# Optimization experiments

Measured on AMD Instinct MI355X. Metric: run time of the kernel, lower is better.

## Reference

```python
import jax, jax.numpy as jnp
import numpy as np

N = 1024
IN_F = 128
H0 = 192  # num_features * 2
H1 = 96   # num_features * 1
BN_EPS = 1e-5
SLOPE = 0.01  # LeakyReLU default negative slope


def setup_inputs() -> dict:
    key = jax.random.key(0)
    ks = jax.random.split(key, 8)
    node_feat = jax.random.normal(ks[0], (N, IN_F), dtype=jnp.float32)
    W0 = jax.random.normal(ks[1], (H0, IN_F), dtype=jnp.float32) * 0.05
    g0 = jnp.ones((H0,), jnp.float32); b0 = jnp.zeros((H0,), jnp.float32)
    m0 = jnp.zeros((H0,), jnp.float32); v0 = jnp.ones((H0,), jnp.float32)
    W1 = jax.random.normal(ks[2], (H1, H0), dtype=jnp.float32) * 0.05
    g1 = jnp.ones((H1,), jnp.float32); b1 = jnp.zeros((H1,), jnp.float32)
    m1 = jnp.zeros((H1,), jnp.float32); v1 = jnp.ones((H1,), jnp.float32)
    Wout = jax.random.normal(ks[3], (1, H1), dtype=jnp.float32) * 0.05
    bout = jnp.zeros((1,), jnp.float32)
    return dict(node_feat=node_feat, W0=W0, g0=g0, b0=b0, m0=m0, v0=v0,
                W1=W1, g1=g1, b1=b1, m1=m1, v1=v1, Wout=Wout, bout=bout)


def _bn(x, g, b, m, v):
    # BatchNorm2d in eval mode over channel axis (last axis here)
    return (x - m) * (g * jax.lax.rsqrt(v + BN_EPS)) + b


def _leaky(x):
    return jnp.where(x >= 0, x, SLOPE * x)


def reference(node_feat, W0, g0, b0, m0, v0, W1, g1, b1, m1, v1, Wout, bout):
    n = node_feat.shape[0]
    # pairwise abs diff: [N, N, F] (symmetric, so torch's i/j transpose is a no-op)
    x_ij = jnp.abs(node_feat[:, None, :] - node_feat[None, :, :])
    # 1x1 convs == per-(i,j) matmuls over channel axis
    h = _leaky(_bn(jnp.einsum('ijf,cf->ijc', x_ij, W0), g0, b0, m0, v0))
    h = _leaky(_bn(jnp.einsum('ijc,dc->ijd', h, W1), g1, b1, m1, v1))
    logits = jnp.einsum('ijd,od->ijo', h, Wout)[..., 0] + bout[0]  # [N, N]
    sim_val = jax.nn.sigmoid(logits)
    edge = sim_val + jnp.eye(n, dtype=sim_val.dtype) + 1e-6
    # torch sums over dim=1 of [1, N, N] -> normalize over the row index i
    edge = edge / jnp.sum(edge, axis=0, keepdims=True)
    return edge[None], sim_val  # edge_feat [1, N, N], sim_val [N, N]
```

## Files before the change

kernel.cpp:

```cpp
#include <hip/hip_runtime.h>
#include <hip/hip_bf16.h>
#include <math.h>

typedef float v4f __attribute__((ext_vector_type(4)));
typedef __bf16 bf16x8 __attribute__((ext_vector_type(8)));
typedef __bf16 bf16x4 __attribute__((ext_vector_type(4)));

#define NN   1024
#define INF  128
#define H0C  192
#define H1C  96

#define WS_W0BF   0
#define WS_W1BF   49152
#define WS_BN0SW  86016
#define WS_BN1SW  86784
#define WS_WOUTSW 87168
#define WS_CINV   87552

__global__ __launch_bounds__(256) void prep_kernel(
    const float* __restrict__ W0, const float* __restrict__ g0,
    const float* __restrict__ b0, const float* __restrict__ m0,
    const float* __restrict__ v0, const float* __restrict__ W1,
    const float* __restrict__ g1, const float* __restrict__ b1,
    const float* __restrict__ m1, const float* __restrict__ v1,
    const float* __restrict__ Wout, char* __restrict__ ws)
{
    int e = blockIdx.x * 256 + threadIdx.x;
    __bf16* w0bf = (__bf16*)(ws + WS_W0BF);
    __bf16* w1bf = (__bf16*)(ws + WS_W1BF);
    float* bn0sw = (float*)(ws + WS_BN0SW);
    float* bn1sw = (float*)(ws + WS_BN1SW);
    float* woutsw = (float*)(ws + WS_WOUTSW);
    if (e < 24576) {
        int j = e & 7, lane = (e >> 3) & 63, t = e >> 9;
        int ks = t & 3, mt = t >> 2;
        int c = mt * 16 + (lane & 15);
        int k = ks * 32 + ((lane >> 4) << 3) + j;
        float s = g0[c] * rsqrtf(v0[c] + 1e-5f);
        w0bf[e] = (__bf16)(W0[c * INF + k] * s);
    } else if (e < 43008) {
        int e2 = e - 24576;
        int j = e2 & 7, lane = (e2 >> 3) & 63, t = e2 >> 9;
        int ks = t % 6, mt = t / 6;
        int c = mt * 16 + (lane & 15);
        int k = ks * 32 + ((lane >> 4) << 3) + j;
        float s = g1[c] * rsqrtf(v1[c] + 1e-5f);
        w1bf[e2] = (__bf16)(W1[c * H0C + k] * s);
    } else if (e < 43200) {
        int e3 = e - 43008;
        int q = e3 / 48, rem = e3 % 48, cm = rem >> 2, r = rem & 3;
        int c = cm * 16 + q * 4 + r;
        float s = g0[c] * rsqrtf(v0[c] + 1e-5f);
        bn0sw[e3] = b0[c] - m0[c] * s;
    } else if (e < 43296) {
        int e4 = e - 43200;
        int q = e4 / 24, rem = e4 % 24, mt = rem >> 2, r = rem & 3;
        int c = mt * 16 + q * 4 + r;
        float s = g1[c] * rsqrtf(v1[c] + 1e-5f);
        bn1sw[e4] = b1[c] - m1[c] * s;
    } else if (e < 43392) {
        int e5 = e - 43296;
        int q = e5 / 24, rem = e5 % 24, mt = rem >> 2, r = rem & 3;
        woutsw[e5] = Wout[mt * 16 + q * 4 + r];
    }
}

__global__ __launch_bounds__(256, 3) void edgenet_main(
    const float* __restrict__ feat, const char* __restrict__ ws,
    const float* __restrict__ boutp, float* __restrict__ sim_out)
{
    __shared__ __align__(16) char smem[51200];
    const int tid = threadIdx.x;
    const int lane = tid & 63;
    const int wave = tid >> 6;
    const int l16 = lane & 15;
    const int quad = lane >> 4;

    const int id = blockIdx.x;
    int bi = (int)((129.0f - sqrtf(16641.0f - 4.0f * (float)id)) * 0.5f);
    while (bi > 0 && bi * (129 - bi) > id) --bi;
    while ((bi + 1) * (128 - bi) <= id) ++bi;
    const int bj = 2 * bi + (id - bi * (129 - bi));
    const int i0 = bi << 4;
    const int j0 = bj << 3;
    const int jb = j0 + wave * 2;

    {
        int ii = tid & 15, fblk = tid >> 4;
        const float* fi = feat + (i0 + ii) * INF + fblk * 8;
        float4 a0 = *(const float4*)fi;
        float4 a1 = *(const float4*)(fi + 4);
        const float* fj = feat + j0 * INF + fblk * 8;
        char* sp = smem + ii * 272 + fblk * 16;
        #pragma unroll
        for (int jj = 0; jj < 8; ++jj) {
            float4 q0 = *(const float4*)fj;
            float4 q1 = *(const float4*)(fj + 4);
            bf16x8 x;
            x[0] = (__bf16)fabsf(a0.x - q0.x);
            x[1] = (__bf16)fabsf(a0.y - q0.y);
            x[2] = (__bf16)fabsf(a0.z - q0.z);
            x[3] = (__bf16)fabsf(a0.w - q0.w);
            x[4] = (__bf16)fabsf(a1.x - q1.x);
            x[5] = (__bf16)fabsf(a1.y - q1.y);
            x[6] = (__bf16)fabsf(a1.z - q1.z);
            x[7] = (__bf16)fabsf(a1.w - q1.w);
            *(bf16x8*)sp = x;
            fj += INF;
            sp += 16 * 272;
        }
    }
    __syncthreads();

    const bf16x8* w0v = (const bf16x8*)(ws + WS_W0BF);
    const bf16x8* w1v = (const bf16x8*)(ws + WS_W1BF);
    const float* bn0sw = (const float*)(ws + WS_BN0SW);
    const float* bn1sw = (const float*)(ws + WS_BN1SW);

    v4f acc1[3][8];
    #pragma unroll
    for (int mt = 0; mt < 3; ++mt) {
        v4f bb = *(const v4f*)(bn0sw + (quad * 12 + wave * 3 + mt) * 4);
        #pragma unroll
        for (int nt = 0; nt < 8; ++nt)
            acc1[mt][nt] = bb;
    }
    #pragma unroll
    for (int ks = 0; ks < 4; ++ks) {
        bf16x8 w[3];
        #pragma unroll
        for (int mt = 0; mt < 3; ++mt)
            w[mt] = w0v[((wave * 3 + mt) * 4 + ks) * 64 + lane];
        #pragma unroll
        for (int nt = 0; nt < 8; ++nt) {
            bf16x8 xk = *(const bf16x8*)(smem +
                (nt * 16 + l16) * 272 + ks * 64 + quad * 16);
            #pragma unroll
            for (int mt = 0; mt < 3; ++mt)
                acc1[mt][nt] = __builtin_amdgcn_mfma_f32_16x16x32_bf16(
                    w[mt], xk, acc1[mt][nt], 0, 0, 0);
        }
    }
    __syncthreads();

    #pragma unroll
    for (int mt = 0; mt < 3; ++mt) {
        int chb = (wave * 3 + mt) * 16 + quad * 4;
        #pragma unroll
        for (int nt = 0; nt < 8; ++nt) {
            bf16x4 pk;
            #pragma unroll
            for (int r = 0; r < 4; ++r) {
                float v = acc1[mt][nt][r];
                v = fmaxf(v, 0.01f * v);
                pk[r] = (__bf16)v;
            }
            *(bf16x4*)(smem + (nt * 16 + l16) * 400 + chb * 2) = pk;
        }
    }
    __syncthreads();

    v4f acc2[6][2];
    #pragma unroll
    for (int mt = 0; mt < 6; ++mt) {
        v4f bb = *(const v4f*)(bn1sw + (quad * 6 + mt) * 4);
        acc2[mt][0] = bb;
        acc2[mt][1] = bb;
    }
    #pragma unroll
    for (int ks = 0; ks < 6; ++ks) {
        bf16x8 h0 = *(const bf16x8*)(smem + ((2 * wave + 0) * 16 + l16) * 400 + ks * 64 + quad * 16);
        bf16x8 h1 = *(const bf16x8*)(smem + ((2 * wave + 1) * 16 + l16) * 400 + ks * 64 + quad * 16);
        #pragma unroll
        for (int mt = 0; mt < 6; ++mt) {
            bf16x8 w = w1v[(mt * 6 + ks) * 64 + lane];
            acc2[mt][0] = __builtin_amdgcn_mfma_f32_16x16x32_bf16(w, h0, acc2[mt][0], 0, 0, 0);
            acc2[mt][1] = __builtin_amdgcn_mfma_f32_16x16x32_bf16(w, h1, acc2[mt][1], 0, 0, 0);
        }
    }

    const float* woutsw = (const float*)(ws + WS_WOUTSW);
    float part[2] = {0.f, 0.f};
    #pragma unroll
    for (int mt = 0; mt < 6; ++mt) {
        v4f wo = *(const v4f*)(woutsw + (quad * 6 + mt) * 4);
        #pragma unroll
        for (int t = 0; t < 2; ++t)
            #pragma unroll
            for (int r = 0; r < 4; ++r) {
                float v = acc2[mt][t][r];
                v = fmaxf(v, 0.01f * v);
                part[t] = fmaf(v, wo[r], part[t]);
            }
    }
    #pragma unroll
    for (int t = 0; t < 2; ++t) {
        part[t] += __shfl_xor(part[t], 16, 64);
        part[t] += __shfl_xor(part[t], 32, 64);
    }
    float z = (quad & 1) ? part[1] : part[0];
    float sv = 1.f / (1.f + expf(-(z + boutp[0])));
    if (quad < 2)
        sim_out[(i0 + l16) * NN + jb + (quad & 1)] = sv;
    else
        sim_out[(jb + (quad & 1)) * NN + i0 + l16] = sv;
}

__global__ __launch_bounds__(256) void cinv_kernel(
    const float* __restrict__ sim, float* __restrict__ cinv)
{
    const int lane = threadIdx.x & 63;
    const int wave = threadIdx.x >> 6;
    const float cadd = 1.0f + (float)NN * 1e-6f;
    #pragma unroll
    for (int rr = 0; rr < 4; ++rr) {
        int j = blockIdx.x * 16 + wave * 4 + rr;
        const float4* row = (const float4*)(sim + j * NN);
        float4 a0 = row[lane];
        float4 a1 = row[lane + 64];
        float4 a2 = row[lane + 128];
        float4 a3 = row[lane + 192];
        float s = (a0.x + a0.y + a0.z + a0.w) + (a1.x + a1.y + a1.z + a1.w)
                + (a2.x + a2.y + a2.z + a2.w) + (a3.x + a3.y + a3.z + a3.w);
        #pragma unroll
        for (int off = 1; off < 64; off <<= 1)
            s += __shfl_xor(s, off, 64);
        if (lane == 0)
            cinv[j] = 1.0f / (s + cadd);
    }
}

__global__ __launch_bounds__(256) void edge_kernel(
    const float* __restrict__ cinv, const float* __restrict__ sim,
    float* __restrict__ edge)
{
    int i = blockIdx.x;
    int jc = threadIdx.x << 2;
    float4 w = *(const float4*)(cinv + jc);
    float4 s = *(const float4*)(sim + i * NN + jc);
    float4 o;
    o.x = (s.x + (i == jc + 0 ? 1.f : 0.f) + 1e-6f) * w.x;
    o.y = (s.y + (i == jc + 1 ? 1.f : 0.f) + 1e-6f) * w.y;
    o.z = (s.z + (i == jc + 2 ? 1.f : 0.f) + 1e-6f) * w.z;
    o.w = (s.w + (i == jc + 3 ? 1.f : 0.f) + 1e-6f) * w.w;
    *(float4*)(edge + i * NN + jc) = o;
}

extern "C" void kernel_launch(void* const* d_in, const int* in_sizes, int n_in,
                              void* d_out, int out_size, void* d_ws, size_t ws_size,
                              hipStream_t stream)
{
    const float* feat = (const float*)d_in[0];
    const float* W0   = (const float*)d_in[1];
    const float* g0   = (const float*)d_in[2];
    const float* b0   = (const float*)d_in[3];
    const float* m0   = (const float*)d_in[4];
    const float* v0   = (const float*)d_in[5];
    const float* W1   = (const float*)d_in[6];
    const float* g1   = (const float*)d_in[7];
    const float* b1   = (const float*)d_in[8];
    const float* m1   = (const float*)d_in[9];
    const float* v1   = (const float*)d_in[10];
    const float* Wout = (const float*)d_in[11];
    const float* bout = (const float*)d_in[12];
    char* ws = (char*)d_ws;
    float* edge = (float*)d_out;
    float* sim  = edge + NN * NN;
    float* cinv = (float*)(ws + WS_CINV);

    prep_kernel<<<dim3(170), dim3(256), 0, stream>>>(
        W0, g0, b0, m0, v0, W1, g1, b1, m1, v1, Wout, ws);
    edgenet_main<<<dim3(4160), dim3(256), 0, stream>>>(feat, ws, bout, sim);
    cinv_kernel<<<dim3(64), dim3(256), 0, stream>>>(sim, cinv);
    edge_kernel<<<dim3(1024), dim3(256), 0, stream>>>(cinv, sim, edge);
}
```

Before: 153.7 us.

## Use six waves per block and split layer-2 work by output channel

Raises the main kernel's block from 4 to 6 waves. Each wave now owns two layer-1 channel tiles and one layer-2 channel tile across all 8 pair tiles. Before, each wave owned three layer-1 tiles and one pair group across all layer-2 channels. Per-wave partial dot products with Wout go through a small shared buffer, are summed by 128 threads after an extra barrier, and are written symmetrically. This lowers per-wave register pressure and accumulator count to raise concurrency, at the cost of an extra sync, more shared memory per block, and fewer resident blocks per CU.

```diff
diff --git a/kernel.cpp b/kernel.cpp
--- a/kernel.cpp
+++ b/kernel.cpp
@@ -66,11 +66,12 @@
     }
 }
 
-__global__ __launch_bounds__(256, 3) void edgenet_main(
+__global__ __launch_bounds__(384, 3) void edgenet_main(
     const float* __restrict__ feat, const char* __restrict__ ws,
     const float* __restrict__ boutp, float* __restrict__ sim_out)
 {
-    __shared__ __align__(16) char smem[51200];
+    __shared__ __align__(16) char smem[54272];
+    float* partial = (float*)(smem + 51200);
     const int tid = threadIdx.x;
     const int lane = tid & 63;
     const int wave = tid >> 6;
@@ -84,32 +85,27 @@
     const int bj = 2 * bi + (id - bi * (129 - bi));
     const int i0 = bi << 4;
     const int j0 = bj << 3;
-    const int jb = j0 + wave * 2;
-
-    {
-        int ii = tid & 15, fblk = tid >> 4;
-        const float* fi = feat + (i0 + ii) * INF + fblk * 8;
+
+    for (int c = tid; c < 2048; c += 384) {
+        int p = c >> 4;
+        int f0 = (c & 15) << 3;
+        int ii = p & 15, jj = p >> 4;
+        const float* fi = feat + (i0 + ii) * INF + f0;
+        const float* fj = feat + (j0 + jj) * INF + f0;
         float4 a0 = *(const float4*)fi;
         float4 a1 = *(const float4*)(fi + 4);
-        const float* fj = feat + j0 * INF + fblk * 8;
-        char* sp = smem + ii * 272 + fblk * 16;
-        #pragma unroll
-        for (int jj = 0; jj < 8; ++jj) {
-            float4 q0 = *(const float4*)fj;
-            float4 q1 = *(const float4*)(fj + 4);
-            bf16x8 x;
-            x[0] = (__bf16)fabsf(a0.x - q0.x);
-            x[1] = (__bf16)fabsf(a0.y - q0.y);
-            x[2] = (__bf16)fabsf(a0.z - q0.z);
-            x[3] = (__bf16)fabsf(a0.w - q0.w);
-            x[4] = (__bf16)fabsf(a1.x - q1.x);
-            x[5] = (__bf16)fabsf(a1.y - q1.y);
-            x[6] = (__bf16)fabsf(a1.z - q1.z);
-            x[7] = (__bf16)fabsf(a1.w - q1.w);
-            *(bf16x8*)sp = x;
-            fj += INF;
-            sp += 16 * 272;
-        }
+        float4 q0 = *(const float4*)fj;
+        float4 q1 = *(const float4*)(fj + 4);
+        bf16x8 x;
+        x[0] = (__bf16)fabsf(a0.x - q0.x);
+        x[1] = (__bf16)fabsf(a0.y - q0.y);
+        x[2] = (__bf16)fabsf(a0.z - q0.z);
+        x[3] = (__bf16)fabsf(a0.w - q0.w);
+        x[4] = (__bf16)fabsf(a1.x - q1.x);
+        x[5] = (__bf16)fabsf(a1.y - q1.y);
+        x[6] = (__bf16)fabsf(a1.z - q1.z);
+        x[7] = (__bf16)fabsf(a1.w - q1.w);
+        *(bf16x8*)(smem + p * 272 + f0 * 2) = x;
     }
     __syncthreads();
 
@@ -118,35 +114,33 @@
     const float* bn0sw = (const float*)(ws + WS_BN0SW);
     const float* bn1sw = (const float*)(ws + WS_BN1SW);
 
-    v4f acc1[3][8];
-    #pragma unroll
-    for (int mt = 0; mt < 3; ++mt) {
-        v4f bb = *(const v4f*)(bn0sw + (quad * 12 + wave * 3 + mt) * 4);
+    v4f acc1[2][8];
+    #pragma unroll
+    for (int mt = 0; mt < 2; ++mt) {
+        v4f bb = *(const v4f*)(bn0sw + (quad * 12 + wave * 2 + mt) * 4);
         #pragma unroll
         for (int nt = 0; nt < 8; ++nt)
             acc1[mt][nt] = bb;
     }
     #pragma unroll
     for (int ks = 0; ks < 4; ++ks) {
-        bf16x8 w[3];
-        #pragma unroll
-        for (int mt = 0; mt < 3; ++mt)
-            w[mt] = w0v[((wave * 3 + mt) * 4 + ks) * 64 + lane];
+        bf16x8 w0a = w0v[((wave * 2 + 0) * 4 + ks) * 64 + lane];
+        bf16x8 w0b = w0v[((wave * 2 + 1) * 4 + ks) * 64 + lane];
         #pragma unroll
         for (int nt = 0; nt < 8; ++nt) {
             bf16x8 xk = *(const bf16x8*)(smem +
                 (nt * 16 + l16) * 272 + ks * 64 + quad * 16);
-            #pragma unroll
-            for (int mt = 0; mt < 3; ++mt)
-                acc1[mt][nt] = __builtin_amdgcn_mfma_f32_16x16x32_bf16(
-                    w[mt], xk, acc1[mt][nt], 0, 0, 0);
-        }
-    }
-    __syncthreads();
-
-    #pragma unroll
-    for (int mt = 0; mt < 3; ++mt) {
-        int chb = (wave * 3 + mt) * 16 + quad * 4;
+            acc1[0][nt] = __builtin_amdgcn_mfma_f32_16x16x32_bf16(
+                w0a, xk, acc1[0][nt], 0, 0, 0);
+            acc1[1][nt] = __builtin_amdgcn_mfma_f32_16x16x32_bf16(
+                w0b, xk, acc1[1][nt], 0, 0, 0);
+        }
+    }
+    __syncthreads();
+
+    #pragma unroll
+    for (int mt = 0; mt < 2; ++mt) {
+        int chb = (wave * 2 + mt) * 16 + quad * 4;
         #pragma unroll
         for (int nt = 0; nt < 8; ++nt) {
             bf16x4 pk;
@@ -161,50 +155,57 @@
     }
     __syncthreads();
 
-    v4f acc2[6][2];
-    #pragma unroll
-    for (int mt = 0; mt < 6; ++mt) {
-        v4f bb = *(const v4f*)(bn1sw + (quad * 6 + mt) * 4);
-        acc2[mt][0] = bb;
-        acc2[mt][1] = bb;
+    v4f acc2[8];
+    {
+        v4f bb = *(const v4f*)(bn1sw + (quad * 6 + wave) * 4);
+        #pragma unroll
+        for (int nt = 0; nt < 8; ++nt)
+            acc2[nt] = bb;
     }
     #pragma unroll
     for (int ks = 0; ks < 6; ++ks) {
-        bf16x8 h0 = *(const bf16x8*)(smem + ((2 * wave + 0) * 16 + l16) * 400 + ks * 64 + quad * 16);
-        bf16x8 h1 = *(const bf16x8*)(smem + ((2 * wave + 1) * 16 + l16) * 400 + ks * 64 + quad * 16);
-        #pragma unroll
-        for (int mt = 0; mt < 6; ++mt) {
-            bf16x8 w = w1v[(mt * 6 + ks) * 64 + lane];
-            acc2[mt][0] = __builtin_amdgcn_mfma_f32_16x16x32_bf16(w, h0, acc2[mt][0], 0, 0, 0);
-            acc2[mt][1] = __builtin_amdgcn_mfma_f32_16x16x32_bf16(w, h1, acc2[mt][1], 0, 0, 0);
+        bf16x8 w = w1v[(wave * 6 + ks) * 64 + lane];
+        #pragma unroll
+        for (int nt = 0; nt < 8; ++nt) {
+            bf16x8 h = *(const bf16x8*)(smem +
+                (nt * 16 + l16) * 400 + ks * 64 + quad * 16);
+            acc2[nt] = __builtin_amdgcn_mfma_f32_16x16x32_bf16(
+                w, h, acc2[nt], 0, 0, 0);
         }
     }
 
     const float* woutsw = (const float*)(ws + WS_WOUTSW);
-    float part[2] = {0.f, 0.f};
-    #pragma unroll
-    for (int mt = 0; mt < 6; ++mt) {
-        v4f wo = *(const v4f*)(woutsw + (quad * 6 + mt) * 4);
-        #pragma unroll
-        for (int t = 0; t < 2; ++t)
-            #pragma unroll
-            for (int r = 0; r < 4; ++r) {
-                float v = acc2[mt][t][r];
-                v = fmaxf(v, 0.01f * v);
-                part[t] = fmaf(v, wo[r], part[t]);
-            }
+    v4f wo = *(const v4f*)(woutsw + (quad * 6 + wave) * 4);
+    float part[8];
+    #pragma unroll
+    for (int nt = 0; nt < 8; ++nt) {
+        float s = 0.f;
+        #pragma unroll
+        for (int r = 0; r < 4; ++r) {
+            float v = acc2[nt][r];
+            v = fmaxf(v, 0.01f * v);
+            s = fmaf(v, wo[r], s);
+        }
+        s += __shfl_xor(s, 16, 64);
+        s += __shfl_xor(s, 32, 64);
+        part[nt] = s;
     }
     #pragma unroll
     for (int t = 0; t < 2; ++t) {
-        part[t] += __shfl_xor(part[t], 16, 64);
-        part[t] += __shfl_xor(part[t], 32, 64);
-    }
-    float z = (quad & 1) ? part[1] : part[0];
-    float sv = 1.f / (1.f + expf(-(z + boutp[0])));
-    if (quad < 2)
-        sim_out[(i0 + l16) * NN + jb + (quad & 1)] = sv;
-    else
-        sim_out[(jb + (quad & 1)) * NN + i0 + l16] = sv;
+        int nt = 2 * quad + t;
+        partial[(nt * 16 + l16) * 6 + wave] = part[nt];
+    }
+    __syncthreads();
+
+    if (tid < 128) {
+        int ii = tid & 15, jj = tid >> 4;
+        float s = partial[tid * 6 + 0] + partial[tid * 6 + 1]
+                + partial[tid * 6 + 2] + partial[tid * 6 + 3]
+                + partial[tid * 6 + 4] + partial[tid * 6 + 5];
+        float sv = 1.f / (1.f + expf(-(s + boutp[0])));
+        sim_out[(i0 + ii) * NN + (j0 + jj)] = sv;
+        sim_out[(j0 + jj) * NN + (i0 + ii)] = sv;
+    }
 }
 
 __global__ __launch_bounds__(256) void cinv_kernel(
@@ -271,7 +272,7 @@
 
     prep_kernel<<<dim3(170), dim3(256), 0, stream>>>(
         W0, g0, b0, m0, v0, W1, g1, b1, m1, v1, Wout, ws);
-    edgenet_main<<<dim3(4160), dim3(256), 0, stream>>>(feat, ws, bout, sim);
+    edgenet_main<<<dim3(4160), dim3(384), 0, stream>>>(feat, ws, bout, sim);
     cinv_kernel<<<dim3(64), dim3(256), 0, stream>>>(sim, cinv);
     edge_kernel<<<dim3(1024), dim3(256), 0, stream>>>(cinv, sim, edge);
 }
```

New measurement: 187.2 us. 1.22x slower.
